# Performance work log

Measured on AMD Instinct MI355X. Metric: run time of the kernel, lower is better.

The kernel has to match this reference:

```python
import jax, jax.numpy as jnp
import numpy as np
from jax import lax

B, C_IN, H, W = 16, 64, 112, 112
OUP = 128
INIT = 64          # ceil(oup/ratio)
NEW = 64           # init*(ratio-1)
E = 4              # num_experts
SE_HID = (INIT + NEW) // 4
EPS = 1e-5


def setup_inputs() -> dict:
    key = jax.random.key(0)
    ks = jax.random.split(key, 12)
    n = jax.random.normal
    d = {}
    d["x"] = n(ks[0], (B, C_IN, H, W), jnp.float32)
    # DynamicConv 1 (1x1, experts)
    d["rw1"] = n(ks[1], (E, C_IN), jnp.float32) * 0.1
    d["rb1"] = jnp.zeros((E,), jnp.float32)
    d["w1"] = n(ks[2], (E, INIT, C_IN, 1, 1), jnp.float32) / np.sqrt(C_IN)
    d["bn1_g"] = jnp.ones((INIT,), jnp.float32)
    d["bn1_b"] = jnp.zeros((INIT,), jnp.float32)
    d["bn1_m"] = n(ks[3], (INIT,), jnp.float32) * 0.1
    d["bn1_v"] = jax.random.uniform(ks[4], (INIT,), jnp.float32, 0.5, 1.5)
    # DynamicConv 2 (3x3 depthwise, experts)
    d["rw2"] = n(ks[5], (E, INIT), jnp.float32) * 0.1
    d["rb2"] = jnp.zeros((E,), jnp.float32)
    d["w2"] = n(ks[6], (E, NEW, 1, 3, 3), jnp.float32) / 3.0
    d["bn2_g"] = jnp.ones((NEW,), jnp.float32)
    d["bn2_b"] = jnp.zeros((NEW,), jnp.float32)
    d["bn2_m"] = n(ks[7], (NEW,), jnp.float32) * 0.1
    d["bn2_v"] = jax.random.uniform(ks[8], (NEW,), jnp.float32, 0.5, 1.5)
    # AdaptiveSE on INIT+NEW channels
    d["se_w1"] = n(ks[9], (SE_HID, INIT + NEW), jnp.float32) * 0.1
    d["se_b1"] = jnp.zeros((SE_HID,), jnp.float32)
    d["se_w2"] = n(ks[10], (INIT + NEW, SE_HID), jnp.float32) * 0.1
    d["se_b2"] = jnp.zeros((INIT + NEW,), jnp.float32)
    return d


def _bn_relu(x, g, b, m, v):
    # eval-mode BatchNorm2d + ReLU, channel dim = 1
    scale = (g / jnp.sqrt(v + EPS))[None, :, None, None]
    shift = (b - m * g / jnp.sqrt(v + EPS))[None, :, None, None]
    return jax.nn.relu(x * scale + shift)


def reference(x, rw1, rb1, w1, bn1_g, bn1_b, bn1_m, bn1_v,
              rw2, rb2, w2, bn2_g, bn2_b, bn2_m, bn2_v,
              se_w1, se_b1, se_w2, se_b2):
    b = x.shape[0]
    # --- first block: dynamic 1x1 conv ---
    pooled = x.mean((2, 3))                                  # [B, C_IN]
    r1 = jax.nn.sigmoid(pooled @ rw1.T + rb1)                # [B, E]
    # per-sample mixed 1x1 kernel: [B, INIT, C_IN]
    k1 = jnp.einsum('be,eoi->boi', r1, w1[:, :, :, 0, 0])
    x1 = jnp.einsum('boi,bihw->bohw', k1, x)                 # [B, INIT, H, W]
    x1 = _bn_relu(x1, bn1_g, bn1_b, bn1_m, bn1_v)
    # --- second block: dynamic 3x3 depthwise conv ---
    pooled2 = x1.mean((2, 3))                                # [B, INIT]
    r2 = jax.nn.sigmoid(pooled2 @ rw2.T + rb2)               # [B, E]
    k2 = jnp.einsum('be,eokl->bokl', r2, w2[:, :, 0])        # [B, NEW, 3, 3]
    # batched grouped conv: groups = B*INIT (CondConv trick)
    x1r = x1.reshape(1, b * INIT, H, W)
    k2r = k2.reshape(b * NEW, 1, 3, 3)
    x2 = lax.conv_general_dilated(
        x1r, k2r, window_strides=(1, 1), padding=((1, 1), (1, 1)),
        dimension_numbers=('NCHW', 'OIHW', 'NCHW'),
        feature_group_count=b * INIT)
    x2 = x2.reshape(b, NEW, H, W)
    x2 = _bn_relu(x2, bn2_g, bn2_b, bn2_m, bn2_v)
    # --- concat + SE gate ---
    out = jnp.concatenate([x1, x2], axis=1)                  # [B, INIT+NEW, H, W]
    s = out.mean((2, 3))                                     # [B, INIT+NEW]
    s = jax.nn.relu(s @ se_w1.T + se_b1)
    s = jax.nn.sigmoid(s @ se_w2.T + se_b2)
    out = out * s[:, :, None, None]
    return out[:, :OUP]
```

## Files before the change

kernel.cpp:

```cpp
#include <hip/hip_runtime.h>
#include <math.h>

#define NB 16
#define CIN 64
#define HH 112
#define WW 112
#define HW 12544
#define INIT_C 64
#define NEW_C 64
#define NE 4
#define SE_HIDN 32
#define OUTC 128
#define EPSV 1e-5f
#define TPX 256
#define NT (HW / TPX)

__global__ __launch_bounds__(256) void k_pool(const float* __restrict__ x,
                                              float* __restrict__ pooled,
                                              float* __restrict__ sum1) {
    int bc = blockIdx.x;
    const float4* p4 = (const float4*)(x + (size_t)bc * HW);
    float s = 0.f;
    for (int g = threadIdx.x; g < HW / 4; g += 256) {
        float4 v = p4[g];
        s += v.x + v.y + v.z + v.w;
    }
    for (int off = 32; off > 0; off >>= 1) s += __shfl_down(s, off, 64);
    __shared__ float ls[4];
    if ((threadIdx.x & 63) == 0) ls[threadIdx.x >> 6] = s;
    __syncthreads();
    if (threadIdx.x == 0) {
        pooled[bc] = (ls[0] + ls[1] + ls[2] + ls[3]) * (1.f / (float)HW);
        sum1[bc] = 0.f;
    }
}

__global__ __launch_bounds__(256) void k_prep(
    const float* __restrict__ pooled, const float* __restrict__ rw1,
    const float* __restrict__ rb1, const float* __restrict__ w1,
    const float* __restrict__ bn1_g, const float* __restrict__ bn1_b,
    const float* __restrict__ bn1_m, const float* __restrict__ bn1_v,
    float* __restrict__ k1t, float* __restrict__ shift1) {
    int b = blockIdx.x;
    int t = threadIdx.x;
    __shared__ float r1s[NE];
    __shared__ float sT[64][65];
    if (t < NE) {
        float acc = rb1[t];
        const float* pb = pooled + b * CIN;
        const float* rw = rw1 + t * CIN;
        for (int i = 0; i < CIN; i++) acc = fmaf(pb[i], rw[i], acc);
        r1s[t] = 1.f / (1.f + expf(-acc));
    }
    if (t >= 64 && t < 128) {
        int o = t - 64;
        float sc = bn1_g[o] * rsqrtf(bn1_v[o] + EPSV);
        shift1[o] = bn1_b[o] - bn1_m[o] * sc;
    }
    __syncthreads();
    for (int idx = t; idx < CIN * INIT_C; idx += 256) {
        int o = idx >> 6, i = idx & 63;
        float acc = 0.f;
#pragma unroll
        for (int e = 0; e < NE; e++)
            acc = fmaf(r1s[e], w1[(e * INIT_C + o) * CIN + i], acc);
        float sc = bn1_g[o] * rsqrtf(bn1_v[o] + EPSV);
        sT[o][i] = acc * sc;
    }
    __syncthreads();
    for (int idx = t; idx < CIN * INIT_C; idx += 256) {
        int i = idx >> 6, o = idx & 63;
        k1t[(b << 12) + idx] = sT[o][i];
    }
}

__global__ __launch_bounds__(256, 4) void k_conv1(
    const float* __restrict__ x, const float* __restrict__ k1t,
    const float* __restrict__ shift1, float* __restrict__ out,
    float* __restrict__ sum1) {
    int b = blockIdx.x / NT;
    int tile = blockIdx.x - b * NT;
    int p0 = tile * TPX;
    int t = threadIdx.x;
    int lane = t & 63;
    int og16 = __builtin_amdgcn_readfirstlane(t >> 6) << 4;
    const float* Aw = k1t + (b << 12) + og16;
    float shv[16];
#pragma unroll
    for (int j = 0; j < 16; j++) shv[j] = shift1[og16 + j];

    const float* xp = x + (size_t)(b * CIN) * HW + p0 + (lane << 2);
    float4 acc[16];
#pragma unroll
    for (int j = 0; j < 16; j++) acc[j] = make_float4(0.f, 0.f, 0.f, 0.f);

#pragma unroll 2
    for (int i = 0; i < CIN; i++) {
        float4 xv = *(const float4*)(xp + (size_t)i * HW);
#pragma unroll
        for (int j = 0; j < 16; j++) {
            float a = Aw[i * 64 + j];
            acc[j].x = fmaf(a, xv.x, acc[j].x);
            acc[j].y = fmaf(a, xv.y, acc[j].y);
            acc[j].z = fmaf(a, xv.z, acc[j].z);
            acc[j].w = fmaf(a, xv.w, acc[j].w);
        }
    }

    float* outbase = out + ((size_t)(b * OUTC + og16)) * HW + p0 + (lane << 2);
#pragma unroll
    for (int j = 0; j < 16; j++) {
        float4 r;
        r.x = fmaxf(acc[j].x + shv[j], 0.f);
        r.y = fmaxf(acc[j].y + shv[j], 0.f);
        r.z = fmaxf(acc[j].z + shv[j], 0.f);
        r.w = fmaxf(acc[j].w + shv[j], 0.f);
        *(float4*)(outbase + (size_t)j * HW) = r;
        float cs = r.x + r.y + r.z + r.w;
        cs += __shfl_xor(cs, 1, 64);
        cs += __shfl_xor(cs, 2, 64);
        cs += __shfl_xor(cs, 4, 64);
        cs += __shfl_xor(cs, 8, 64);
        cs += __shfl_xor(cs, 16, 64);
        cs += __shfl_xor(cs, 32, 64);
        if (lane == 0) atomicAdd(&sum1[b * INIT_C + og16 + j], cs);
    }
}

__device__ __forceinline__ void ldrow(const float* __restrict__ sP, int pr,
                                      int cg, float4& C, float& L, float& R) {
    const float* row = sP + pr * WW;
    C = *(const float4*)(row + cg * 4);
    int lc = cg * 4 - 1;
    lc = lc < 0 ? 0 : lc;
    float lv = row[lc];
    L = (cg == 0) ? 0.f : lv;
    int rc = cg * 4 + 4;
    rc = rc > (WW - 1) ? (WW - 1) : rc;
    float rv = row[rc];
    R = (cg == 27) ? 0.f : rv;
}

__device__ __forceinline__ float4 dw9(const float4 c0, float l0, float r0,
                                      const float4 c1, float l1, float r1,
                                      const float4 c2, float l2, float r2,
                                      const float* __restrict__ K) {
    float4 o;
    o.x = fmaf(K[0], l0, fmaf(K[1], c0.x, fmaf(K[2], c0.y,
          fmaf(K[3], l1, fmaf(K[4], c1.x, fmaf(K[5], c1.y,
          fmaf(K[6], l2, fmaf(K[7], c2.x, K[8] * c2.y))))))));
    o.y = fmaf(K[0], c0.x, fmaf(K[1], c0.y, fmaf(K[2], c0.z,
          fmaf(K[3], c1.x, fmaf(K[4], c1.y, fmaf(K[5], c1.z,
          fmaf(K[6], c2.x, fmaf(K[7], c2.y, K[8] * c2.z))))))));
    o.z = fmaf(K[0], c0.y, fmaf(K[1], c0.z, fmaf(K[2], c0.w,
          fmaf(K[3], c1.y, fmaf(K[4], c1.z, fmaf(K[5], c1.w,
          fmaf(K[6], c2.y, fmaf(K[7], c2.z, K[8] * c2.w))))))));
    o.w = fmaf(K[0], c0.z, fmaf(K[1], c0.w, fmaf(K[2], r0,
          fmaf(K[3], c1.z, fmaf(K[4], c1.w, fmaf(K[5], r1,
          fmaf(K[6], c2.z, fmaf(K[7], c2.w, K[8] * r2))))))));
    return o;
}

#define PROWS (HH + 2)

__global__ __launch_bounds__(256) void k_dwsum(
    const float* __restrict__ xin, const float* __restrict__ sum1,
    const float* __restrict__ rw2, const float* __restrict__ rb2,
    const float* __restrict__ w2, const float* __restrict__ bn2_g,
    const float* __restrict__ bn2_b, const float* __restrict__ bn2_m,
    const float* __restrict__ bn2_v, float* __restrict__ sum2) {
    __shared__ alignas(16) float sP[PROWS * WW];
    __shared__ float r2s[NE];
    __shared__ float kks[9];
    int c = blockIdx.x & 63;
    int b = blockIdx.x >> 6;
    int t = threadIdx.x;

    if (t < NE) {
        float acc = rb2[t];
        const float* s1 = sum1 + b * INIT_C;
        const float* rw = rw2 + t * INIT_C;
        for (int i = 0; i < INIT_C; i++)
            acc = fmaf(s1[i] * (1.f / (float)HW), rw[i], acc);
        r2s[t] = 1.f / (1.f + expf(-acc));
    }
    if (t < WW / 4) {
        float4 z = {0.f, 0.f, 0.f, 0.f};
        ((float4*)sP)[t] = z;
        ((float4*)(sP + (PROWS - 1) * WW))[t] = z;
    }
    __syncthreads();
    if (t < 9) {
        float acc = 0.f;
#pragma unroll
        for (int e = 0; e < NE; e++)
            acc = fmaf(r2s[e], w2[(e * NEW_C + c) * 9 + t], acc);
        kks[t] = acc * (bn2_g[c] * rsqrtf(bn2_v[c] + EPSV));
    }
    const float4* src4 = (const float4*)(xin + ((size_t)(b * OUTC + c)) * HW);
    float4* dst4 = (float4*)(sP + WW);
    for (int g = t; g < HW / 4; g += 256) dst4[g] = src4[g];
    __syncthreads();

    float sc2 = bn2_g[c] * rsqrtf(bn2_v[c] + EPSV);
    float shift = bn2_b[c] - bn2_m[c] * sc2;
    float myk[9];
#pragma unroll
    for (int j = 0; j < 9; j++) myk[j] = kks[j];

    int cg = t & 31;
    int band = t >> 5;
    float csum = 0.f;
    if (cg < 28) {
        int pr0 = band * 14;
        float4 C[3];
        float L[3], R[3];
        ldrow(sP, pr0, cg, C[0], L[0], R[0]);
        ldrow(sP, pr0 + 1, cg, C[1], L[1], R[1]);
#pragma unroll
        for (int k = 0; k < 14; k++) {
            int s0 = k % 3, s1 = (k + 1) % 3, s2 = (k + 2) % 3;
            ldrow(sP, pr0 + k + 2, cg, C[s2], L[s2], R[s2]);
            float4 o = dw9(C[s0], L[s0], R[s0], C[s1], L[s1], R[s1],
                           C[s2], L[s2], R[s2], myk);
            csum += fmaxf(o.x + shift, 0.f) + fmaxf(o.y + shift, 0.f) +
                    fmaxf(o.z + shift, 0.f) + fmaxf(o.w + shift, 0.f);
        }
    }
    for (int off = 32; off > 0; off >>= 1) csum += __shfl_down(csum, off, 64);
    __shared__ float ls[4];
    if ((t & 63) == 0) ls[t >> 6] = csum;
    __syncthreads();
    if (t == 0) sum2[b * NEW_C + c] = ls[0] + ls[1] + ls[2] + ls[3];
}

__global__ __launch_bounds__(256) void k_final(
    const float* __restrict__ xin, const float* __restrict__ sum1,
    const float* __restrict__ sum2, const float* __restrict__ rw2,
    const float* __restrict__ rb2, const float* __restrict__ w2,
    const float* __restrict__ bn2_g, const float* __restrict__ bn2_b,
    const float* __restrict__ bn2_m, const float* __restrict__ bn2_v,
    const float* __restrict__ se_w1, const float* __restrict__ se_b1,
    const float* __restrict__ se_w2, const float* __restrict__ se_b2,
    float* __restrict__ out) {
    __shared__ alignas(16) float sP[PROWS * WW];
    __shared__ float sin_[OUTC];
    __shared__ float hvec[SE_HIDN];
    __shared__ float r2s[NE];
    __shared__ float kks[9];
    int c = blockIdx.x & 63;
    int b = blockIdx.x >> 6;
    int t = threadIdx.x;

    if (t < 64) sin_[t] = sum1[b * 64 + t] * (1.f / (float)HW);
    else if (t < 128) sin_[t] = sum2[b * 64 + (t - 64)] * (1.f / (float)HW);
    if (t >= 128 && t < 128 + NE) {
        int e = t - 128;
        float acc = rb2[e];
        const float* s1 = sum1 + b * INIT_C;
        const float* rw = rw2 + e * INIT_C;
        for (int i = 0; i < INIT_C; i++)
            acc = fmaf(s1[i] * (1.f / (float)HW), rw[i], acc);
        r2s[e] = 1.f / (1.f + expf(-acc));
    }
    if (t >= 160 && t < 160 + WW / 4) {
        float4 z = {0.f, 0.f, 0.f, 0.f};
        ((float4*)sP)[t - 160] = z;
        ((float4*)(sP + (PROWS - 1) * WW))[t - 160] = z;
    }
    __syncthreads();
    if (t < SE_HIDN) {
        float acc = se_b1[t];
        const float* wrow = se_w1 + t * OUTC;
#pragma unroll 4
        for (int i = 0; i < OUTC; i++) acc = fmaf(sin_[i], wrow[i], acc);
        hvec[t] = fmaxf(acc, 0.f);
    }
    if (t >= 64 && t < 73) {
        int j = t - 64;
        float acc = 0.f;
#pragma unroll
        for (int e = 0; e < NE; e++)
            acc = fmaf(r2s[e], w2[(e * NEW_C + c) * 9 + j], acc);
        kks[j] = acc * (bn2_g[c] * rsqrtf(bn2_v[c] + EPSV));
    }
    const float4* src4 = (const float4*)(xin + ((size_t)(b * OUTC + c)) * HW);
    float4* pdst4 = (float4*)(sP + WW);
    for (int g = t; g < HW / 4; g += 256) pdst4[g] = src4[g];
    __syncthreads();
    float a1 = se_b2[c], a2 = se_b2[64 + c];
    {
        const float* w2a = se_w2 + c * SE_HIDN;
        const float* w2b = se_w2 + (64 + c) * SE_HIDN;
#pragma unroll 8
        for (int j = 0; j < SE_HIDN; j++) {
            float hj = hvec[j];
            a1 = fmaf(hj, w2a[j], a1);
            a2 = fmaf(hj, w2b[j], a2);
        }
    }
    float s1v = 1.f / (1.f + expf(-a1));
    float s2v = 1.f / (1.f + expf(-a2));
    float sc2 = bn2_g[c] * rsqrtf(bn2_v[c] + EPSV);
    float shift = bn2_b[c] - bn2_m[c] * sc2;
    float myk[9];
#pragma unroll
    for (int j = 0; j < 9; j++) myk[j] = kks[j];

    int cg = t & 31;
    int band = t >> 5;
    if (cg < 28) {
        float* d1 = out + ((size_t)(b * OUTC + c)) * HW;
        float* d2 = out + ((size_t)(b * OUTC + 64 + c)) * HW;
        int pr0 = band * 14;
        float4 C[3];
        float L[3], R[3];
        ldrow(sP, pr0, cg, C[0], L[0], R[0]);
        ldrow(sP, pr0 + 1, cg, C[1], L[1], R[1]);
#pragma unroll
        for (int k = 0; k < 14; k++) {
            int s0 = k % 3, s1 = (k + 1) % 3, s2 = (k + 2) % 3;
            ldrow(sP, pr0 + k + 2, cg, C[s2], L[s2], R[s2]);
            float4 o = dw9(C[s0], L[s0], R[s0], C[s1], L[s1], R[s1],
                           C[s2], L[s2], R[s2], myk);
            float4 x1v = C[s1];
            float4 o1, o2;
            o1.x = x1v.x * s1v; o1.y = x1v.y * s1v;
            o1.z = x1v.z * s1v; o1.w = x1v.w * s1v;
            o2.x = fmaxf(o.x + shift, 0.f) * s2v;
            o2.y = fmaxf(o.y + shift, 0.f) * s2v;
            o2.z = fmaxf(o.z + shift, 0.f) * s2v;
            o2.w = fmaxf(o.w + shift, 0.f) * s2v;
            int row = band * 14 + k;
            *(float4*)(d1 + (size_t)row * WW + cg * 4) = o1;
            *(float4*)(d2 + (size_t)row * WW + cg * 4) = o2;
        }
    }
}

extern "C" void kernel_launch(void* const* d_in, const int* in_sizes, int n_in,
                              void* d_out, int out_size, void* d_ws,
                              size_t ws_size, hipStream_t stream) {
    (void)in_sizes; (void)n_in; (void)out_size; (void)ws_size;
    const float* x = (const float*)d_in[0];
    const float* rw1 = (const float*)d_in[1];
    const float* rb1 = (const float*)d_in[2];
    const float* w1 = (const float*)d_in[3];
    const float* bn1_g = (const float*)d_in[4];
    const float* bn1_b = (const float*)d_in[5];
    const float* bn1_m = (const float*)d_in[6];
    const float* bn1_v = (const float*)d_in[7];
    const float* rw2 = (const float*)d_in[8];
    const float* rb2 = (const float*)d_in[9];
    const float* w2 = (const float*)d_in[10];
    const float* bn2_g = (const float*)d_in[11];
    const float* bn2_b = (const float*)d_in[12];
    const float* bn2_m = (const float*)d_in[13];
    const float* bn2_v = (const float*)d_in[14];
    const float* se_w1 = (const float*)d_in[15];
    const float* se_b1 = (const float*)d_in[16];
    const float* se_w2 = (const float*)d_in[17];
    const float* se_b2 = (const float*)d_in[18];
    float* out = (float*)d_out;
    float* ws = (float*)d_ws;
    float* pooled = ws;
    float* sum1 = ws + 1024;
    float* sum2 = ws + 2048;
    float* shift1 = ws + 3072;
    float* k1t = ws + 4096;

    k_pool<<<NB * CIN, 256, 0, stream>>>(x, pooled, sum1);
    k_prep<<<NB, 256, 0, stream>>>(pooled, rw1, rb1, w1, bn1_g, bn1_b, bn1_m,
                                   bn1_v, k1t, shift1);
    k_conv1<<<NB * NT, 256, 0, stream>>>(x, k1t, shift1, out, sum1);
    k_dwsum<<<NB * NEW_C, 256, 0, stream>>>(out, sum1, rw2, rb2, w2, bn2_g,
                                            bn2_b, bn2_m, bn2_v, sum2);
    k_final<<<NB * NEW_C, 256, 0, stream>>>(out, sum1, sum2, rw2, rb2, w2,
                                            bn2_g, bn2_b, bn2_m, bn2_v, se_w1,
                                            se_b1, se_w2, se_b2, out);
}
```

Baseline: 285.3 us.

## Fuse all stages into one cooperative persistent kernel with grid syncs

Replaces the five separate launches (pool, prep, 1x1 conv, depthwise-sum, final SE/depthwise) with a single cooperative kernel of 1024 blocks that separates the phases with grid.sync. The depthwise stage now works in two 56-row halves and keeps the lower half of each x1 channel in LDS. The final phase reuses that half directly and saves the boundary row before overwriting, so only the upper half is re-read from global memory. The aim is to remove inter-kernel launch gaps and some x1 re-read traffic. In exchange it pays for grid-wide barriers and needs all blocks co-resident, falling back to the old multi-kernel path if the cooperative launch fails.

```diff
diff --git a/kernel.cpp b/kernel.cpp
--- a/kernel.cpp
+++ b/kernel.cpp
@@ -1,5 +1,8 @@
 #include <hip/hip_runtime.h>
+#include <hip/hip_cooperative_groups.h>
 #include <math.h>
+
+namespace cgrp = cooperative_groups;
 
 #define NB 16
 #define CIN 64
@@ -14,6 +17,326 @@
 #define EPSV 1e-5f
 #define TPX 256
 #define NT (HW / TPX)
+#define NTILE (NB * NT)
+#define GRID 1024
+#define CHR 56
+#define SROWS (CHR + 2)
+
+__device__ __forceinline__ void ldrow(const float* sP, int pr, int cq,
+                                      float4& C, float& L, float& R) {
+    const float* row = sP + pr * WW;
+    C = *(const float4*)(row + cq * 4);
+    int lc = cq * 4 - 1;
+    lc = lc < 0 ? 0 : lc;
+    float lv = row[lc];
+    L = (cq == 0) ? 0.f : lv;
+    int rc = cq * 4 + 4;
+    rc = rc > (WW - 1) ? (WW - 1) : rc;
+    float rv = row[rc];
+    R = (cq == 27) ? 0.f : rv;
+}
+
+__device__ __forceinline__ float4 dw9(const float4 c0, float l0, float r0,
+                                      const float4 c1, float l1, float r1,
+                                      const float4 c2, float l2, float r2,
+                                      const float* K) {
+    float4 o;
+    o.x = fmaf(K[0], l0, fmaf(K[1], c0.x, fmaf(K[2], c0.y,
+          fmaf(K[3], l1, fmaf(K[4], c1.x, fmaf(K[5], c1.y,
+          fmaf(K[6], l2, fmaf(K[7], c2.x, K[8] * c2.y))))))));
+    o.y = fmaf(K[0], c0.x, fmaf(K[1], c0.y, fmaf(K[2], c0.z,
+          fmaf(K[3], c1.x, fmaf(K[4], c1.y, fmaf(K[5], c1.z,
+          fmaf(K[6], c2.x, fmaf(K[7], c2.y, K[8] * c2.z))))))));
+    o.z = fmaf(K[0], c0.y, fmaf(K[1], c0.z, fmaf(K[2], c0.w,
+          fmaf(K[3], c1.y, fmaf(K[4], c1.z, fmaf(K[5], c1.w,
+          fmaf(K[6], c2.y, fmaf(K[7], c2.z, K[8] * c2.w))))))));
+    o.w = fmaf(K[0], c0.z, fmaf(K[1], c0.w, fmaf(K[2], r0,
+          fmaf(K[3], c1.z, fmaf(K[4], c1.w, fmaf(K[5], r1,
+          fmaf(K[6], c2.z, fmaf(K[7], c2.w, K[8] * r2))))))));
+    return o;
+}
+
+__global__ __launch_bounds__(256, 4) void k_fused(
+    const float* x, const float* rw1, const float* rb1, const float* w1,
+    const float* bn1_g, const float* bn1_b, const float* bn1_m,
+    const float* bn1_v, const float* rw2, const float* rb2, const float* w2,
+    const float* bn2_g, const float* bn2_b, const float* bn2_m,
+    const float* bn2_v, const float* se_w1, const float* se_b1,
+    const float* se_w2, const float* se_b2, float* out, float* pooled,
+    float* sum1, float* sum2, float* shift1, float* k1t) {
+    cgrp::grid_group grid = cgrp::this_grid();
+    __shared__ alignas(16) float sPc[SROWS * WW];
+    __shared__ alignas(16) float srow56[WW];
+    __shared__ float sinv[OUTC];
+    __shared__ float hvec[SE_HIDN];
+    __shared__ float sc4[NE];
+    __shared__ float kks[9];
+    __shared__ float lred[4];
+
+    int t = threadIdx.x;
+    int blk = blockIdx.x;
+
+    {
+        const float4* p4 = (const float4*)(x + (size_t)blk * HW);
+        float s = 0.f;
+        for (int g = t; g < HW / 4; g += 256) {
+            float4 v = p4[g];
+            s += v.x + v.y + v.z + v.w;
+        }
+        for (int off = 32; off > 0; off >>= 1) s += __shfl_down(s, off, 64);
+        if ((t & 63) == 0) lred[t >> 6] = s;
+        __syncthreads();
+        if (t == 0) {
+            pooled[blk] = (lred[0] + lred[1] + lred[2] + lred[3]) *
+                          (1.f / (float)HW);
+            sum1[blk] = 0.f;
+        }
+    }
+    grid.sync();
+
+    if (blk < NB) {
+        int b = blk;
+        if (t < NE) {
+            float acc = rb1[t];
+            const float* pb = pooled + b * CIN;
+            const float* rw = rw1 + t * CIN;
+            for (int i = 0; i < CIN; i++) acc = fmaf(pb[i], rw[i], acc);
+            sc4[t] = 1.f / (1.f + expf(-acc));
+        }
+        if (t >= 64 && t < 128) {
+            int o = t - 64;
+            float sc = bn1_g[o] * rsqrtf(bn1_v[o] + EPSV);
+            shift1[o] = bn1_b[o] - bn1_m[o] * sc;
+        }
+        __syncthreads();
+        float* sT = sPc;
+        for (int idx = t; idx < CIN * INIT_C; idx += 256) {
+            int o = idx >> 6, i = idx & 63;
+            float acc = 0.f;
+#pragma unroll
+            for (int e = 0; e < NE; e++)
+                acc = fmaf(sc4[e], w1[(e * INIT_C + o) * CIN + i], acc);
+            float sc = bn1_g[o] * rsqrtf(bn1_v[o] + EPSV);
+            sT[o * 65 + i] = acc * sc;
+        }
+        __syncthreads();
+        for (int idx = t; idx < CIN * INIT_C; idx += 256) {
+            int i = idx >> 6, o = idx & 63;
+            k1t[(b << 12) + idx] = sT[o * 65 + i];
+        }
+    }
+    grid.sync();
+
+    for (int task = blk; task < NTILE; task += GRID) {
+        int b = task / NT;
+        int tile = task - b * NT;
+        int p0 = tile * TPX;
+        int lane = t & 63;
+        int og16 = __builtin_amdgcn_readfirstlane(t >> 6) << 4;
+        const float* Aw = k1t + (b << 12) + og16;
+        const float* xp = x + (size_t)(b * CIN) * HW + p0 + (lane << 2);
+        float4 acc[16];
+#pragma unroll
+        for (int j = 0; j < 16; j++) acc[j] = make_float4(0.f, 0.f, 0.f, 0.f);
+#pragma unroll 2
+        for (int i = 0; i < CIN; i++) {
+            float4 xv = *(const float4*)(xp + (size_t)i * HW);
+#pragma unroll
+            for (int j = 0; j < 16; j++) {
+                float a = Aw[i * 64 + j];
+                acc[j].x = fmaf(a, xv.x, acc[j].x);
+                acc[j].y = fmaf(a, xv.y, acc[j].y);
+                acc[j].z = fmaf(a, xv.z, acc[j].z);
+                acc[j].w = fmaf(a, xv.w, acc[j].w);
+            }
+        }
+        float* outbase =
+            out + ((size_t)(b * OUTC + og16)) * HW + p0 + (lane << 2);
+#pragma unroll
+        for (int j = 0; j < 16; j++) {
+            float sh = shift1[og16 + j];
+            float4 r;
+            r.x = fmaxf(acc[j].x + sh, 0.f);
+            r.y = fmaxf(acc[j].y + sh, 0.f);
+            r.z = fmaxf(acc[j].z + sh, 0.f);
+            r.w = fmaxf(acc[j].w + sh, 0.f);
+            *(float4*)(outbase + (size_t)j * HW) = r;
+            float cs = r.x + r.y + r.z + r.w;
+            cs += __shfl_xor(cs, 1, 64);
+            cs += __shfl_xor(cs, 2, 64);
+            cs += __shfl_xor(cs, 4, 64);
+            cs += __shfl_xor(cs, 8, 64);
+            cs += __shfl_xor(cs, 16, 64);
+            cs += __shfl_xor(cs, 32, 64);
+            if (lane == 0) atomicAdd(&sum1[b * INIT_C + og16 + j], cs);
+        }
+    }
+    grid.sync();
+
+    int c = blk & 63;
+    int b = blk >> 6;
+    {
+        if (t < NE) {
+            float acc = rb2[t];
+            const float* s1 = sum1 + b * INIT_C;
+            const float* rw = rw2 + t * INIT_C;
+            for (int i = 0; i < INIT_C; i++)
+                acc = fmaf(s1[i] * (1.f / (float)HW), rw[i], acc);
+            sc4[t] = 1.f / (1.f + expf(-acc));
+        }
+        __syncthreads();
+        if (t < 9) {
+            float acc = 0.f;
+#pragma unroll
+            for (int e = 0; e < NE; e++)
+                acc = fmaf(sc4[e], w2[(e * NEW_C + c) * 9 + t], acc);
+            kks[t] = acc * (bn2_g[c] * rsqrtf(bn2_v[c] + EPSV));
+        }
+        __syncthreads();
+        float sc2 = bn2_g[c] * rsqrtf(bn2_v[c] + EPSV);
+        float shift2 = bn2_b[c] - bn2_m[c] * sc2;
+        float myk[9];
+#pragma unroll
+        for (int j = 0; j < 9; j++) myk[j] = kks[j];
+        const float* xsrc = out + ((size_t)(b * OUTC + c)) * HW;
+        int cq = t & 31, band = t >> 5;
+        float csum = 0.f;
+        for (int ch = 0; ch < 2; ch++) {
+            int h0 = ch * CHR;
+            __syncthreads();
+            for (int g = t; g < SROWS * 28; g += 256) {
+                int r = g / 28, cc = g - r * 28;
+                int gr = h0 - 1 + r;
+                float4 v = make_float4(0.f, 0.f, 0.f, 0.f);
+                if (gr >= 0 && gr < HH)
+                    v = *(const float4*)(xsrc + (size_t)gr * WW + (cc << 2));
+                ((float4*)sPc)[g] = v;
+            }
+            __syncthreads();
+            if (cq < 28) {
+                int j0 = band * 7;
+                float4 C[3];
+                float L[3], R[3];
+                ldrow(sPc, j0, cq, C[0], L[0], R[0]);
+                ldrow(sPc, j0 + 1, cq, C[1], L[1], R[1]);
+#pragma unroll
+                for (int k = 0; k < 7; k++) {
+                    int s0 = k % 3, s1i = (k + 1) % 3, s2i = (k + 2) % 3;
+                    ldrow(sPc, j0 + k + 2, cq, C[s2i], L[s2i], R[s2i]);
+                    float4 o = dw9(C[s0], L[s0], R[s0], C[s1i], L[s1i], R[s1i],
+                                   C[s2i], L[s2i], R[s2i], myk);
+                    csum += fmaxf(o.x + shift2, 0.f) + fmaxf(o.y + shift2, 0.f) +
+                            fmaxf(o.z + shift2, 0.f) + fmaxf(o.w + shift2, 0.f);
+                }
+            }
+        }
+        for (int off = 32; off > 0; off >>= 1) csum += __shfl_down(csum, off, 64);
+        if ((t & 63) == 0) lred[t >> 6] = csum;
+        __syncthreads();
+        if (t == 0) sum2[blk] = lred[0] + lred[1] + lred[2] + lred[3];
+    }
+    grid.sync();
+
+    {
+        int cq = t & 31, band = t >> 5;
+        if (t < 64) sinv[t] = sum1[b * 64 + t] * (1.f / (float)HW);
+        else if (t < 128) sinv[t] = sum2[b * 64 + (t - 64)] * (1.f / (float)HW);
+        if (t >= 128 && t < 156)
+            ((float4*)srow56)[t - 128] = ((const float4*)(sPc + WW))[t - 128];
+        __syncthreads();
+        if (t < SE_HIDN) {
+            float acc = se_b1[t];
+            const float* wrow = se_w1 + t * OUTC;
+#pragma unroll 4
+            for (int i = 0; i < OUTC; i++) acc = fmaf(sinv[i], wrow[i], acc);
+            hvec[t] = fmaxf(acc, 0.f);
+        }
+        __syncthreads();
+        float a1 = se_b2[c], a2 = se_b2[64 + c];
+        {
+            const float* w2a = se_w2 + c * SE_HIDN;
+            const float* w2b = se_w2 + (64 + c) * SE_HIDN;
+#pragma unroll 8
+            for (int j = 0; j < SE_HIDN; j++) {
+                float hj = hvec[j];
+                a1 = fmaf(hj, w2a[j], a1);
+                a2 = fmaf(hj, w2b[j], a2);
+            }
+        }
+        float s1v = 1.f / (1.f + expf(-a1));
+        float s2v = 1.f / (1.f + expf(-a2));
+        float sc2 = bn2_g[c] * rsqrtf(bn2_v[c] + EPSV);
+        float shift2 = bn2_b[c] - bn2_m[c] * sc2;
+        float myk[9];
+#pragma unroll
+        for (int j = 0; j < 9; j++) myk[j] = kks[j];
+        float* d1 = out + ((size_t)(b * OUTC + c)) * HW;
+        float* d2 = out + ((size_t)(b * OUTC + 64 + c)) * HW;
+
+        if (cq < 28) {
+            int j0 = band * 7;
+            float4 C[3];
+            float L[3], R[3];
+            ldrow(sPc, j0, cq, C[0], L[0], R[0]);
+            ldrow(sPc, j0 + 1, cq, C[1], L[1], R[1]);
+#pragma unroll
+            for (int k = 0; k < 7; k++) {
+                int s0 = k % 3, s1i = (k + 1) % 3, s2i = (k + 2) % 3;
+                ldrow(sPc, j0 + k + 2, cq, C[s2i], L[s2i], R[s2i]);
+                float4 o = dw9(C[s0], L[s0], R[s0], C[s1i], L[s1i], R[s1i],
+                               C[s2i], L[s2i], R[s2i], myk);
+                float4 x1v = C[s1i];
+                float4 o1, o2;
+                o1.x = x1v.x * s1v; o1.y = x1v.y * s1v;
+                o1.z = x1v.z * s1v; o1.w = x1v.w * s1v;
+                o2.x = fmaxf(o.x + shift2, 0.f) * s2v;
+                o2.y = fmaxf(o.y + shift2, 0.f) * s2v;
+                o2.z = fmaxf(o.z + shift2, 0.f) * s2v;
+                o2.w = fmaxf(o.w + shift2, 0.f) * s2v;
+                int row = CHR + j0 + k;
+                *(float4*)(d1 + (size_t)row * WW + cq * 4) = o1;
+                *(float4*)(d2 + (size_t)row * WW + cq * 4) = o2;
+            }
+        }
+        __syncthreads();
+        for (int g = t; g < SROWS * 28; g += 256) {
+            int r = g / 28, cc = g - r * 28;
+            int gr = r - 1;
+            float4 v = make_float4(0.f, 0.f, 0.f, 0.f);
+            if (gr >= 0 && gr < CHR)
+                v = *(const float4*)(d1 + (size_t)gr * WW + (cc << 2));
+            else if (gr == CHR)
+                v = ((const float4*)srow56)[cc];
+            ((float4*)sPc)[g] = v;
+        }
+        __syncthreads();
+        if (cq < 28) {
+            int j0 = band * 7;
+            float4 C[3];
+            float L[3], R[3];
+            ldrow(sPc, j0, cq, C[0], L[0], R[0]);
+            ldrow(sPc, j0 + 1, cq, C[1], L[1], R[1]);
+#pragma unroll
+            for (int k = 0; k < 7; k++) {
+                int s0 = k % 3, s1i = (k + 1) % 3, s2i = (k + 2) % 3;
+                ldrow(sPc, j0 + k + 2, cq, C[s2i], L[s2i], R[s2i]);
+                float4 o = dw9(C[s0], L[s0], R[s0], C[s1i], L[s1i], R[s1i],
+                               C[s2i], L[s2i], R[s2i], myk);
+                float4 x1v = C[s1i];
+                float4 o1, o2;
+                o1.x = x1v.x * s1v; o1.y = x1v.y * s1v;
+                o1.z = x1v.z * s1v; o1.w = x1v.w * s1v;
+                o2.x = fmaxf(o.x + shift2, 0.f) * s2v;
+                o2.y = fmaxf(o.y + shift2, 0.f) * s2v;
+                o2.z = fmaxf(o.z + shift2, 0.f) * s2v;
+                o2.w = fmaxf(o.w + shift2, 0.f) * s2v;
+                int row = j0 + k;
+                *(float4*)(d1 + (size_t)row * WW + cq * 4) = o1;
+                *(float4*)(d2 + (size_t)row * WW + cq * 4) = o2;
+            }
+        }
+    }
+}
 
 __global__ __launch_bounds__(256) void k_pool(const float* __restrict__ x,
                                               float* __restrict__ pooled,
@@ -85,15 +408,10 @@
     int lane = t & 63;
     int og16 = __builtin_amdgcn_readfirstlane(t >> 6) << 4;
     const float* Aw = k1t + (b << 12) + og16;
-    float shv[16];
-#pragma unroll
-    for (int j = 0; j < 16; j++) shv[j] = shift1[og16 + j];
-
     const float* xp = x + (size_t)(b * CIN) * HW + p0 + (lane << 2);
     float4 acc[16];
 #pragma unroll
     for (int j = 0; j < 16; j++) acc[j] = make_float4(0.f, 0.f, 0.f, 0.f);
-
 #pragma unroll 2
     for (int i = 0; i < CIN; i++) {
         float4 xv = *(const float4*)(xp + (size_t)i * HW);
@@ -106,15 +424,15 @@
             acc[j].w = fmaf(a, xv.w, acc[j].w);
         }
     }
-
     float* outbase = out + ((size_t)(b * OUTC + og16)) * HW + p0 + (lane << 2);
 #pragma unroll
     for (int j = 0; j < 16; j++) {
+        float sh = shift1[og16 + j];
         float4 r;
-        r.x = fmaxf(acc[j].x + shv[j], 0.f);
-        r.y = fmaxf(acc[j].y + shv[j], 0.f);
-        r.z = fmaxf(acc[j].z + shv[j], 0.f);
-        r.w = fmaxf(acc[j].w + shv[j], 0.f);
+        r.x = fmaxf(acc[j].x + sh, 0.f);
+        r.y = fmaxf(acc[j].y + sh, 0.f);
+        r.z = fmaxf(acc[j].z + sh, 0.f);
+        r.w = fmaxf(acc[j].w + sh, 0.f);
         *(float4*)(outbase + (size_t)j * HW) = r;
         float cs = r.x + r.y + r.z + r.w;
         cs += __shfl_xor(cs, 1, 64);
@@ -125,40 +443,6 @@
         cs += __shfl_xor(cs, 32, 64);
         if (lane == 0) atomicAdd(&sum1[b * INIT_C + og16 + j], cs);
     }
-}
-
-__device__ __forceinline__ void ldrow(const float* __restrict__ sP, int pr,
-                                      int cg, float4& C, float& L, float& R) {
-    const float* row = sP + pr * WW;
-    C = *(const float4*)(row + cg * 4);
-    int lc = cg * 4 - 1;
-    lc = lc < 0 ? 0 : lc;
-    float lv = row[lc];
-    L = (cg == 0) ? 0.f : lv;
-    int rc = cg * 4 + 4;
-    rc = rc > (WW - 1) ? (WW - 1) : rc;
-    float rv = row[rc];
-    R = (cg == 27) ? 0.f : rv;
-}
-
-__device__ __forceinline__ float4 dw9(const float4 c0, float l0, float r0,
-                                      const float4 c1, float l1, float r1,
-                                      const float4 c2, float l2, float r2,
-                                      const float* __restrict__ K) {
-    float4 o;
-    o.x = fmaf(K[0], l0, fmaf(K[1], c0.x, fmaf(K[2], c0.y,
-          fmaf(K[3], l1, fmaf(K[4], c1.x, fmaf(K[5], c1.y,
-          fmaf(K[6], l2, fmaf(K[7], c2.x, K[8] * c2.y))))))));
-    o.y = fmaf(K[0], c0.x, fmaf(K[1], c0.y, fmaf(K[2], c0.z,
-          fmaf(K[3], c1.x, fmaf(K[4], c1.y, fmaf(K[5], c1.z,
-          fmaf(K[6], c2.x, fmaf(K[7], c2.y, K[8] * c2.z))))))));
-    o.z = fmaf(K[0], c0.y, fmaf(K[1], c0.z, fmaf(K[2], c0.w,
-          fmaf(K[3], c1.y, fmaf(K[4], c1.z, fmaf(K[5], c1.w,
-          fmaf(K[6], c2.y, fmaf(K[7], c2.z, K[8] * c2.w))))))));
-    o.w = fmaf(K[0], c0.z, fmaf(K[1], c0.w, fmaf(K[2], r0,
-          fmaf(K[3], c1.z, fmaf(K[4], c1.w, fmaf(K[5], r1,
-          fmaf(K[6], c2.z, fmaf(K[7], c2.w, K[8] * r2))))))));
-    return o;
 }
 
 #define PROWS (HH + 2)
@@ -175,7 +459,6 @@
     int c = blockIdx.x & 63;
     int b = blockIdx.x >> 6;
     int t = threadIdx.x;
-
     if (t < NE) {
         float acc = rb2[t];
         const float* s1 = sum1 + b * INIT_C;
@@ -201,28 +484,26 @@
     float4* dst4 = (float4*)(sP + WW);
     for (int g = t; g < HW / 4; g += 256) dst4[g] = src4[g];
     __syncthreads();
-
     float sc2 = bn2_g[c] * rsqrtf(bn2_v[c] + EPSV);
     float shift = bn2_b[c] - bn2_m[c] * sc2;
     float myk[9];
 #pragma unroll
     for (int j = 0; j < 9; j++) myk[j] = kks[j];
-
-    int cg = t & 31;
+    int cq = t & 31;
     int band = t >> 5;
     float csum = 0.f;
-    if (cg < 28) {
+    if (cq < 28) {
         int pr0 = band * 14;
         float4 C[3];
         float L[3], R[3];
-        ldrow(sP, pr0, cg, C[0], L[0], R[0]);
-        ldrow(sP, pr0 + 1, cg, C[1], L[1], R[1]);
+        ldrow(sP, pr0, cq, C[0], L[0], R[0]);
+        ldrow(sP, pr0 + 1, cq, C[1], L[1], R[1]);
 #pragma unroll
         for (int k = 0; k < 14; k++) {
             int s0 = k % 3, s1 = (k + 1) % 3, s2 = (k + 2) % 3;
-            ldrow(sP, pr0 + k + 2, cg, C[s2], L[s2], R[s2]);
-            float4 o = dw9(C[s0], L[s0], R[s0], C[s1], L[s1], R[s1],
-                           C[s2], L[s2], R[s2], myk);
+            ldrow(sP, pr0 + k + 2, cq, C[s2], L[s2], R[s2]);
+            float4 o = dw9(C[s0], L[s0], R[s0], C[s1], L[s1], R[s1], C[s2],
+                           L[s2], R[s2], myk);
             csum += fmaxf(o.x + shift, 0.f) + fmaxf(o.y + shift, 0.f) +
                     fmaxf(o.z + shift, 0.f) + fmaxf(o.w + shift, 0.f);
         }
@@ -251,7 +532,6 @@
     int c = blockIdx.x & 63;
     int b = blockIdx.x >> 6;
     int t = threadIdx.x;
-
     if (t < 64) sin_[t] = sum1[b * 64 + t] * (1.f / (float)HW);
     else if (t < 128) sin_[t] = sum2[b * 64 + (t - 64)] * (1.f / (float)HW);
     if (t >= 128 && t < 128 + NE) {
@@ -306,23 +586,22 @@
     float myk[9];
 #pragma unroll
     for (int j = 0; j < 9; j++) myk[j] = kks[j];
-
-    int cg = t & 31;
+    int cq = t & 31;
     int band = t >> 5;
-    if (cg < 28) {
+    if (cq < 28) {
         float* d1 = out + ((size_t)(b * OUTC + c)) * HW;
         float* d2 = out + ((size_t)(b * OUTC + 64 + c)) * HW;
         int pr0 = band * 14;
         float4 C[3];
         float L[3], R[3];
-        ldrow(sP, pr0, cg, C[0], L[0], R[0]);
-        ldrow(sP, pr0 + 1, cg, C[1], L[1], R[1]);
+        ldrow(sP, pr0, cq, C[0], L[0], R[0]);
+        ldrow(sP, pr0 + 1, cq, C[1], L[1], R[1]);
 #pragma unroll
         for (int k = 0; k < 14; k++) {
             int s0 = k % 3, s1 = (k + 1) % 3, s2 = (k + 2) % 3;
-            ldrow(sP, pr0 + k + 2, cg, C[s2], L[s2], R[s2]);
-            float4 o = dw9(C[s0], L[s0], R[s0], C[s1], L[s1], R[s1],
-                           C[s2], L[s2], R[s2], myk);
+            ldrow(sP, pr0 + k + 2, cq, C[s2], L[s2], R[s2]);
+            float4 o = dw9(C[s0], L[s0], R[s0], C[s1], L[s1], R[s1], C[s2],
+                           L[s2], R[s2], myk);
             float4 x1v = C[s1];
             float4 o1, o2;
             o1.x = x1v.x * s1v; o1.y = x1v.y * s1v;
@@ -332,8 +611,8 @@
             o2.z = fmaxf(o.z + shift, 0.f) * s2v;
             o2.w = fmaxf(o.w + shift, 0.f) * s2v;
             int row = band * 14 + k;
-            *(float4*)(d1 + (size_t)row * WW + cg * 4) = o1;
-            *(float4*)(d2 + (size_t)row * WW + cg * 4) = o2;
+            *(float4*)(d1 + (size_t)row * WW + cq * 4) = o1;
+            *(float4*)(d2 + (size_t)row * WW + cq * 4) = o2;
         }
     }
 }
@@ -369,13 +648,25 @@
     float* shift1 = ws + 3072;
     float* k1t = ws + 4096;
 
-    k_pool<<<NB * CIN, 256, 0, stream>>>(x, pooled, sum1);
-    k_prep<<<NB, 256, 0, stream>>>(pooled, rw1, rb1, w1, bn1_g, bn1_b, bn1_m,
-                                   bn1_v, k1t, shift1);
-    k_conv1<<<NB * NT, 256, 0, stream>>>(x, k1t, shift1, out, sum1);
-    k_dwsum<<<NB * NEW_C, 256, 0, stream>>>(out, sum1, rw2, rb2, w2, bn2_g,
-                                            bn2_b, bn2_m, bn2_v, sum2);
-    k_final<<<NB * NEW_C, 256, 0, stream>>>(out, sum1, sum2, rw2, rb2, w2,
-                                            bn2_g, bn2_b, bn2_m, bn2_v, se_w1,
-                                            se_b1, se_w2, se_b2, out);
-}
+    void* kargs[] = {
+        (void*)&x,     (void*)&rw1,   (void*)&rb1,    (void*)&w1,
+        (void*)&bn1_g, (void*)&bn1_b, (void*)&bn1_m,  (void*)&bn1_v,
+        (void*)&rw2,   (void*)&rb2,   (void*)&w2,     (void*)&bn2_g,
+        (void*)&bn2_b, (void*)&bn2_m, (void*)&bn2_v,  (void*)&se_w1,
+        (void*)&se_b1, (void*)&se_w2, (void*)&se_b2,  (void*)&out,
+        (void*)&pooled,(void*)&sum1,  (void*)&sum2,   (void*)&shift1,
+        (void*)&k1t};
+    hipError_t e = hipLaunchCooperativeKernel((void*)k_fused, dim3(GRID),
+                                              dim3(256), kargs, 0, stream);
+    if (e != hipSuccess) {
+        k_pool<<<NB * CIN, 256, 0, stream>>>(x, pooled, sum1);
+        k_prep<<<NB, 256, 0, stream>>>(pooled, rw1, rb1, w1, bn1_g, bn1_b,
+                                       bn1_m, bn1_v, k1t, shift1);
+        k_conv1<<<NB * NT, 256, 0, stream>>>(x, k1t, shift1, out, sum1);
+        k_dwsum<<<NB * NEW_C, 256, 0, stream>>>(out, sum1, rw2, rb2, w2, bn2_g,
+                                                bn2_b, bn2_m, bn2_v, sum2);
+        k_final<<<NB * NEW_C, 256, 0, stream>>>(out, sum1, sum2, rw2, rb2, w2,
+                                                bn2_g, bn2_b, bn2_m, bn2_v,
+                                                se_w1, se_b1, se_w2, se_b2, out);
+    }
+}
```

Result: slower. 719.4 us (+152.1%).

## Split depthwise stages into half-image chunks to cut LDS and raise occupancy

Applied to the files above, without the earlier changes.

The depthwise-sum and final kernels now stage half of each 112x112 channel plane (58 padded rows) in LDS per pass instead of the whole plane, with in-bounds zero padding replacing the separate halo fill. This roughly halves shared memory per block so more blocks fit per CU. The final kernel processes the bottom half first, saves the boundary row, then reloads the top half, because it overwrites its input in place. Output stores become nontemporal, and conv1 unrolls the channel loop further and loads the BN shift late to save registers. The in-place ordering is delicate, and the extra barriers and reloads add some overhead.

```diff
diff --git a/kernel.cpp b/kernel.cpp
--- a/kernel.cpp
+++ b/kernel.cpp
@@ -14,6 +14,16 @@
 #define EPSV 1e-5f
 #define TPX 256
 #define NT (HW / TPX)
+#define CHR 56
+#define SROWS (CHR + 2)
+
+typedef float nf4 __attribute__((ext_vector_type(4)));
+
+__device__ __forceinline__ void nt_store4(float* p, float a, float b, float c,
+                                          float d) {
+    nf4 v = {a, b, c, d};
+    __builtin_nontemporal_store(v, (nf4*)p);
+}
 
 __global__ __launch_bounds__(256) void k_pool(const float* __restrict__ x,
                                               float* __restrict__ pooled,
@@ -85,16 +95,11 @@
     int lane = t & 63;
     int og16 = __builtin_amdgcn_readfirstlane(t >> 6) << 4;
     const float* Aw = k1t + (b << 12) + og16;
-    float shv[16];
-#pragma unroll
-    for (int j = 0; j < 16; j++) shv[j] = shift1[og16 + j];
-
     const float* xp = x + (size_t)(b * CIN) * HW + p0 + (lane << 2);
     float4 acc[16];
 #pragma unroll
     for (int j = 0; j < 16; j++) acc[j] = make_float4(0.f, 0.f, 0.f, 0.f);
-
-#pragma unroll 2
+#pragma unroll 4
     for (int i = 0; i < CIN; i++) {
         float4 xv = *(const float4*)(xp + (size_t)i * HW);
 #pragma unroll
@@ -106,15 +111,15 @@
             acc[j].w = fmaf(a, xv.w, acc[j].w);
         }
     }
-
     float* outbase = out + ((size_t)(b * OUTC + og16)) * HW + p0 + (lane << 2);
 #pragma unroll
     for (int j = 0; j < 16; j++) {
+        float sh = shift1[og16 + j];
         float4 r;
-        r.x = fmaxf(acc[j].x + shv[j], 0.f);
-        r.y = fmaxf(acc[j].y + shv[j], 0.f);
-        r.z = fmaxf(acc[j].z + shv[j], 0.f);
-        r.w = fmaxf(acc[j].w + shv[j], 0.f);
+        r.x = fmaxf(acc[j].x + sh, 0.f);
+        r.y = fmaxf(acc[j].y + sh, 0.f);
+        r.z = fmaxf(acc[j].z + sh, 0.f);
+        r.w = fmaxf(acc[j].w + sh, 0.f);
         *(float4*)(outbase + (size_t)j * HW) = r;
         float cs = r.x + r.y + r.z + r.w;
         cs += __shfl_xor(cs, 1, 64);
@@ -127,24 +132,24 @@
     }
 }
 
-__device__ __forceinline__ void ldrow(const float* __restrict__ sP, int pr,
-                                      int cg, float4& C, float& L, float& R) {
+__device__ __forceinline__ void ldrow(const float* sP, int pr, int cq,
+                                      float4& C, float& L, float& R) {
     const float* row = sP + pr * WW;
-    C = *(const float4*)(row + cg * 4);
-    int lc = cg * 4 - 1;
+    C = *(const float4*)(row + cq * 4);
+    int lc = cq * 4 - 1;
     lc = lc < 0 ? 0 : lc;
     float lv = row[lc];
-    L = (cg == 0) ? 0.f : lv;
-    int rc = cg * 4 + 4;
+    L = (cq == 0) ? 0.f : lv;
+    int rc = cq * 4 + 4;
     rc = rc > (WW - 1) ? (WW - 1) : rc;
     float rv = row[rc];
-    R = (cg == 27) ? 0.f : rv;
+    R = (cq == 27) ? 0.f : rv;
 }
 
 __device__ __forceinline__ float4 dw9(const float4 c0, float l0, float r0,
                                       const float4 c1, float l1, float r1,
                                       const float4 c2, float l2, float r2,
-                                      const float* __restrict__ K) {
+                                      const float* K) {
     float4 o;
     o.x = fmaf(K[0], l0, fmaf(K[1], c0.x, fmaf(K[2], c0.y,
           fmaf(K[3], l1, fmaf(K[4], c1.x, fmaf(K[5], c1.y,
@@ -161,17 +166,16 @@
     return o;
 }
 
-#define PROWS (HH + 2)
-
 __global__ __launch_bounds__(256) void k_dwsum(
     const float* __restrict__ xin, const float* __restrict__ sum1,
     const float* __restrict__ rw2, const float* __restrict__ rb2,
     const float* __restrict__ w2, const float* __restrict__ bn2_g,
     const float* __restrict__ bn2_b, const float* __restrict__ bn2_m,
     const float* __restrict__ bn2_v, float* __restrict__ sum2) {
-    __shared__ alignas(16) float sP[PROWS * WW];
+    __shared__ alignas(16) float sP[SROWS * WW];
     __shared__ float r2s[NE];
     __shared__ float kks[9];
+    __shared__ float lred[4];
     int c = blockIdx.x & 63;
     int b = blockIdx.x >> 6;
     int t = threadIdx.x;
@@ -184,11 +188,6 @@
             acc = fmaf(s1[i] * (1.f / (float)HW), rw[i], acc);
         r2s[t] = 1.f / (1.f + expf(-acc));
     }
-    if (t < WW / 4) {
-        float4 z = {0.f, 0.f, 0.f, 0.f};
-        ((float4*)sP)[t] = z;
-        ((float4*)(sP + (PROWS - 1) * WW))[t] = z;
-    }
     __syncthreads();
     if (t < 9) {
         float acc = 0.f;
@@ -197,54 +196,62 @@
             acc = fmaf(r2s[e], w2[(e * NEW_C + c) * 9 + t], acc);
         kks[t] = acc * (bn2_g[c] * rsqrtf(bn2_v[c] + EPSV));
     }
-    const float4* src4 = (const float4*)(xin + ((size_t)(b * OUTC + c)) * HW);
-    float4* dst4 = (float4*)(sP + WW);
-    for (int g = t; g < HW / 4; g += 256) dst4[g] = src4[g];
-    __syncthreads();
-
+    __syncthreads();
     float sc2 = bn2_g[c] * rsqrtf(bn2_v[c] + EPSV);
-    float shift = bn2_b[c] - bn2_m[c] * sc2;
+    float shift2 = bn2_b[c] - bn2_m[c] * sc2;
     float myk[9];
 #pragma unroll
     for (int j = 0; j < 9; j++) myk[j] = kks[j];
 
-    int cg = t & 31;
-    int band = t >> 5;
+    const float* xsrc = xin + ((size_t)(b * OUTC + c)) * HW;
+    int cq = t & 31, band = t >> 5;
     float csum = 0.f;
-    if (cg < 28) {
-        int pr0 = band * 14;
-        float4 C[3];
-        float L[3], R[3];
-        ldrow(sP, pr0, cg, C[0], L[0], R[0]);
-        ldrow(sP, pr0 + 1, cg, C[1], L[1], R[1]);
-#pragma unroll
-        for (int k = 0; k < 14; k++) {
-            int s0 = k % 3, s1 = (k + 1) % 3, s2 = (k + 2) % 3;
-            ldrow(sP, pr0 + k + 2, cg, C[s2], L[s2], R[s2]);
-            float4 o = dw9(C[s0], L[s0], R[s0], C[s1], L[s1], R[s1],
-                           C[s2], L[s2], R[s2], myk);
-            csum += fmaxf(o.x + shift, 0.f) + fmaxf(o.y + shift, 0.f) +
-                    fmaxf(o.z + shift, 0.f) + fmaxf(o.w + shift, 0.f);
+    for (int ch = 0; ch < 2; ch++) {
+        int h0 = ch * CHR;
+        __syncthreads();
+        for (int g = t; g < SROWS * 28; g += 256) {
+            int r = g / 28, cc = g - r * 28;
+            int gr = h0 - 1 + r;
+            float4 v = make_float4(0.f, 0.f, 0.f, 0.f);
+            if (gr >= 0 && gr < HH)
+                v = *(const float4*)(xsrc + (size_t)gr * WW + (cc << 2));
+            ((float4*)sP)[g] = v;
+        }
+        __syncthreads();
+        if (cq < 28) {
+            int j0 = band * 7;
+            float4 C[3];
+            float L[3], R[3];
+            ldrow(sP, j0, cq, C[0], L[0], R[0]);
+            ldrow(sP, j0 + 1, cq, C[1], L[1], R[1]);
+#pragma unroll
+            for (int k = 0; k < 7; k++) {
+                int s0 = k % 3, s1i = (k + 1) % 3, s2i = (k + 2) % 3;
+                ldrow(sP, j0 + k + 2, cq, C[s2i], L[s2i], R[s2i]);
+                float4 o = dw9(C[s0], L[s0], R[s0], C[s1i], L[s1i], R[s1i],
+                               C[s2i], L[s2i], R[s2i], myk);
+                csum += fmaxf(o.x + shift2, 0.f) + fmaxf(o.y + shift2, 0.f) +
+                        fmaxf(o.z + shift2, 0.f) + fmaxf(o.w + shift2, 0.f);
+            }
         }
     }
     for (int off = 32; off > 0; off >>= 1) csum += __shfl_down(csum, off, 64);
-    __shared__ float ls[4];
-    if ((t & 63) == 0) ls[t >> 6] = csum;
-    __syncthreads();
-    if (t == 0) sum2[b * NEW_C + c] = ls[0] + ls[1] + ls[2] + ls[3];
+    if ((t & 63) == 0) lred[t >> 6] = csum;
+    __syncthreads();
+    if (t == 0) sum2[blockIdx.x] = lred[0] + lred[1] + lred[2] + lred[3];
 }
 
 __global__ __launch_bounds__(256) void k_final(
-    const float* __restrict__ xin, const float* __restrict__ sum1,
-    const float* __restrict__ sum2, const float* __restrict__ rw2,
-    const float* __restrict__ rb2, const float* __restrict__ w2,
-    const float* __restrict__ bn2_g, const float* __restrict__ bn2_b,
-    const float* __restrict__ bn2_m, const float* __restrict__ bn2_v,
-    const float* __restrict__ se_w1, const float* __restrict__ se_b1,
-    const float* __restrict__ se_w2, const float* __restrict__ se_b2,
-    float* __restrict__ out) {
-    __shared__ alignas(16) float sP[PROWS * WW];
-    __shared__ float sin_[OUTC];
+    const float* __restrict__ sum1, const float* __restrict__ sum2,
+    const float* __restrict__ rw2, const float* __restrict__ rb2,
+    const float* __restrict__ w2, const float* __restrict__ bn2_g,
+    const float* __restrict__ bn2_b, const float* __restrict__ bn2_m,
+    const float* __restrict__ bn2_v, const float* __restrict__ se_w1,
+    const float* __restrict__ se_b1, const float* __restrict__ se_w2,
+    const float* __restrict__ se_b2, float* __restrict__ out) {
+    __shared__ alignas(16) float sP[SROWS * WW];
+    __shared__ alignas(16) float srow56[WW];
+    __shared__ float sinv[OUTC];
     __shared__ float hvec[SE_HIDN];
     __shared__ float r2s[NE];
     __shared__ float kks[9];
@@ -252,8 +259,8 @@
     int b = blockIdx.x >> 6;
     int t = threadIdx.x;
 
-    if (t < 64) sin_[t] = sum1[b * 64 + t] * (1.f / (float)HW);
-    else if (t < 128) sin_[t] = sum2[b * 64 + (t - 64)] * (1.f / (float)HW);
+    if (t < 64) sinv[t] = sum1[b * 64 + t] * (1.f / (float)HW);
+    else if (t < 128) sinv[t] = sum2[b * 64 + (t - 64)] * (1.f / (float)HW);
     if (t >= 128 && t < 128 + NE) {
         int e = t - 128;
         float acc = rb2[e];
@@ -263,17 +270,12 @@
             acc = fmaf(s1[i] * (1.f / (float)HW), rw[i], acc);
         r2s[e] = 1.f / (1.f + expf(-acc));
     }
-    if (t >= 160 && t < 160 + WW / 4) {
-        float4 z = {0.f, 0.f, 0.f, 0.f};
-        ((float4*)sP)[t - 160] = z;
-        ((float4*)(sP + (PROWS - 1) * WW))[t - 160] = z;
-    }
     __syncthreads();
     if (t < SE_HIDN) {
         float acc = se_b1[t];
         const float* wrow = se_w1 + t * OUTC;
 #pragma unroll 4
-        for (int i = 0; i < OUTC; i++) acc = fmaf(sin_[i], wrow[i], acc);
+        for (int i = 0; i < OUTC; i++) acc = fmaf(sinv[i], wrow[i], acc);
         hvec[t] = fmaxf(acc, 0.f);
     }
     if (t >= 64 && t < 73) {
@@ -284,10 +286,17 @@
             acc = fmaf(r2s[e], w2[(e * NEW_C + c) * 9 + j], acc);
         kks[j] = acc * (bn2_g[c] * rsqrtf(bn2_v[c] + EPSV));
     }
-    const float4* src4 = (const float4*)(xin + ((size_t)(b * OUTC + c)) * HW);
-    float4* pdst4 = (float4*)(sP + WW);
-    for (int g = t; g < HW / 4; g += 256) pdst4[g] = src4[g];
-    __syncthreads();
+    float* d1 = out + ((size_t)(b * OUTC + c)) * HW;
+    float* d2 = out + ((size_t)(b * OUTC + 64 + c)) * HW;
+    for (int g = t; g < SROWS * 28; g += 256) {
+        int r = g / 28, cc = g - r * 28;
+        int gr = CHR - 1 + r;
+        float4 v = make_float4(0.f, 0.f, 0.f, 0.f);
+        if (gr < HH) v = *(const float4*)(d1 + (size_t)gr * WW + (cc << 2));
+        ((float4*)sP)[g] = v;
+    }
+    __syncthreads();
+    if (t < 28) ((float4*)srow56)[t] = ((const float4*)(sP + WW))[t];
     float a1 = se_b2[c], a2 = se_b2[64 + c];
     {
         const float* w2a = se_w2 + c * SE_HIDN;
@@ -302,38 +311,68 @@
     float s1v = 1.f / (1.f + expf(-a1));
     float s2v = 1.f / (1.f + expf(-a2));
     float sc2 = bn2_g[c] * rsqrtf(bn2_v[c] + EPSV);
-    float shift = bn2_b[c] - bn2_m[c] * sc2;
+    float shift2 = bn2_b[c] - bn2_m[c] * sc2;
     float myk[9];
 #pragma unroll
     for (int j = 0; j < 9; j++) myk[j] = kks[j];
 
-    int cg = t & 31;
-    int band = t >> 5;
-    if (cg < 28) {
-        float* d1 = out + ((size_t)(b * OUTC + c)) * HW;
-        float* d2 = out + ((size_t)(b * OUTC + 64 + c)) * HW;
-        int pr0 = band * 14;
+    int cq = t & 31, band = t >> 5;
+    if (cq < 28) {
+        int j0 = band * 7;
         float4 C[3];
         float L[3], R[3];
-        ldrow(sP, pr0, cg, C[0], L[0], R[0]);
-        ldrow(sP, pr0 + 1, cg, C[1], L[1], R[1]);
-#pragma unroll
-        for (int k = 0; k < 14; k++) {
-            int s0 = k % 3, s1 = (k + 1) % 3, s2 = (k + 2) % 3;
-            ldrow(sP, pr0 + k + 2, cg, C[s2], L[s2], R[s2]);
-            float4 o = dw9(C[s0], L[s0], R[s0], C[s1], L[s1], R[s1],
-                           C[s2], L[s2], R[s2], myk);
-            float4 x1v = C[s1];
-            float4 o1, o2;
-            o1.x = x1v.x * s1v; o1.y = x1v.y * s1v;
-            o1.z = x1v.z * s1v; o1.w = x1v.w * s1v;
-            o2.x = fmaxf(o.x + shift, 0.f) * s2v;
-            o2.y = fmaxf(o.y + shift, 0.f) * s2v;
-            o2.z = fmaxf(o.z + shift, 0.f) * s2v;
-            o2.w = fmaxf(o.w + shift, 0.f) * s2v;
-            int row = band * 14 + k;
-            *(float4*)(d1 + (size_t)row * WW + cg * 4) = o1;
-            *(float4*)(d2 + (size_t)row * WW + cg * 4) = o2;
+        ldrow(sP, j0, cq, C[0], L[0], R[0]);
+        ldrow(sP, j0 + 1, cq, C[1], L[1], R[1]);
+#pragma unroll
+        for (int k = 0; k < 7; k++) {
+            int s0 = k % 3, s1i = (k + 1) % 3, s2i = (k + 2) % 3;
+            ldrow(sP, j0 + k + 2, cq, C[s2i], L[s2i], R[s2i]);
+            float4 o = dw9(C[s0], L[s0], R[s0], C[s1i], L[s1i], R[s1i],
+                           C[s2i], L[s2i], R[s2i], myk);
+            float4 x1v = C[s1i];
+            int row = CHR + j0 + k;
+            nt_store4(d1 + (size_t)row * WW + cq * 4, x1v.x * s1v, x1v.y * s1v,
+                      x1v.z * s1v, x1v.w * s1v);
+            nt_store4(d2 + (size_t)row * WW + cq * 4,
+                      fmaxf(o.x + shift2, 0.f) * s2v,
+                      fmaxf(o.y + shift2, 0.f) * s2v,
+                      fmaxf(o.z + shift2, 0.f) * s2v,
+                      fmaxf(o.w + shift2, 0.f) * s2v);
+        }
+    }
+    __syncthreads();
+    for (int g = t; g < SROWS * 28; g += 256) {
+        int r = g / 28, cc = g - r * 28;
+        int gr = r - 1;
+        float4 v = make_float4(0.f, 0.f, 0.f, 0.f);
+        if (gr >= 0 && gr < CHR)
+            v = *(const float4*)(d1 + (size_t)gr * WW + (cc << 2));
+        else if (gr == CHR)
+            v = ((const float4*)srow56)[cc];
+        ((float4*)sP)[g] = v;
+    }
+    __syncthreads();
+    if (cq < 28) {
+        int j0 = band * 7;
+        float4 C[3];
+        float L[3], R[3];
+        ldrow(sP, j0, cq, C[0], L[0], R[0]);
+        ldrow(sP, j0 + 1, cq, C[1], L[1], R[1]);
+#pragma unroll
+        for (int k = 0; k < 7; k++) {
+            int s0 = k % 3, s1i = (k + 1) % 3, s2i = (k + 2) % 3;
+            ldrow(sP, j0 + k + 2, cq, C[s2i], L[s2i], R[s2i]);
+            float4 o = dw9(C[s0], L[s0], R[s0], C[s1i], L[s1i], R[s1i],
+                           C[s2i], L[s2i], R[s2i], myk);
+            float4 x1v = C[s1i];
+            int row = j0 + k;
+            nt_store4(d1 + (size_t)row * WW + cq * 4, x1v.x * s1v, x1v.y * s1v,
+                      x1v.z * s1v, x1v.w * s1v);
+            nt_store4(d2 + (size_t)row * WW + cq * 4,
+                      fmaxf(o.x + shift2, 0.f) * s2v,
+                      fmaxf(o.y + shift2, 0.f) * s2v,
+                      fmaxf(o.z + shift2, 0.f) * s2v,
+                      fmaxf(o.w + shift2, 0.f) * s2v);
         }
     }
 }
@@ -375,7 +414,7 @@
     k_conv1<<<NB * NT, 256, 0, stream>>>(x, k1t, shift1, out, sum1);
     k_dwsum<<<NB * NEW_C, 256, 0, stream>>>(out, sum1, rw2, rb2, w2, bn2_g,
                                             bn2_b, bn2_m, bn2_v, sum2);
-    k_final<<<NB * NEW_C, 256, 0, stream>>>(out, sum1, sum2, rw2, rb2, w2,
-                                            bn2_g, bn2_b, bn2_m, bn2_v, se_w1,
-                                            se_b1, se_w2, se_b2, out);
-}
+    k_final<<<NB * NEW_C, 256, 0, stream>>>(sum1, sum2, rw2, rb2, w2, bn2_g,
+                                            bn2_b, bn2_m, bn2_v, se_w1, se_b1,
+                                            se_w2, se_b2, out);
+}
```

Result: faster. 279.5 us (-2.0%).
